# Performance work log

Measured on AMD Instinct MI355X. Metric: run time of the kernel, lower is better.

The kernel has to match this reference:

```python
import jax, jax.numpy as jnp
import numpy as np

SEQ, B, V, E, H, L = 64, 64, 32000, 512, 512, 2


def setup_inputs() -> dict:
    key = jax.random.key(0)
    ks = jax.random.split(key, 12)
    k = float(np.sqrt(1.0 / H))
    u = lambda kk, shape, a, b: jax.random.uniform(kk, shape, jnp.float32, a, b)
    return {
        "inputs": jax.random.randint(ks[0], (SEQ, B), 0, V),          # [T, B] token ids
        "hidden": jnp.zeros((L, B, H), jnp.float32),                   # initial hidden
        "emb": u(ks[1], (V, E), -0.1, 0.1),                            # embedding table
        "Wr_w": u(ks[2], (L, H, E + H), -k, k),                        # reset gate [L,H,2H]
        "Wr_b": u(ks[3], (L, H), -k, k),
        "Wz_w": u(ks[4], (L, H, E + H), -k, k),                        # update gate
        "Wz_b": u(ks[5], (L, H), -k, k),
        "Wh_w": u(ks[6], (L, H, E + H), -k, k),                        # candidate
        "Wh_b": u(ks[7], (L, H), -k, k),
        "out_w": u(ks[8], (V, H), -0.1, 0.1),                          # output projection
        "out_b": jnp.zeros((V,), jnp.float32),
    }


def reference(inputs, hidden, emb, Wr_w, Wr_b, Wz_w, Wz_b, Wh_w, Wh_b, out_w, out_b):
    # GRU recurrence over time via lax.scan (dropout disabled: dp_keep_prob=1.0)
    def step(h, tok):
        x = emb[tok]  # [B, E]
        new_h = []
        for i in range(L):  # fixed small layer loop
            hi = h[i]  # [B, H]
            cat = jnp.concatenate([x, hi], axis=1)  # [B, E+H]
            r = jax.nn.sigmoid(cat @ Wr_w[i].T + Wr_b[i])
            z = jax.nn.sigmoid(cat @ Wz_w[i].T + Wz_b[i])
            h_hat = jnp.tanh(jnp.concatenate([x, r * hi], axis=1) @ Wh_w[i].T + Wh_b[i])
            x = (1.0 - z) * hi + z * h_hat  # next layer input / new hidden
            new_h.append(x)
        logits_t = x @ out_w.T + out_b  # [B, V]
        return jnp.stack(new_h), logits_t

    hidden_final, logits = jax.lax.scan(step, hidden, inputs)
    return logits, hidden_final  # [T,B,V], [L,B,H]
```

## Files before the change

kernel.cpp:

```cpp
#include <hip/hip_runtime.h>

constexpr int NT = 64;
constexpr int NB = 64;
constexpr int NV = 32000;
constexpr int NE = 512;
constexpr int NH = 512;
constexpr int NPAIR = 16 * 250;

constexpr size_t SZ_OW  = (size_t)NV * NE;
constexpr size_t SZ_XE  = (size_t)NT * NB * NE;
constexpr size_t SZ_H   = (size_t)NB * NH;
constexpr size_t LOGITS = (size_t)NT * NB * NV;

typedef float f32x4 __attribute__((ext_vector_type(4)));
typedef int   i32x4 __attribute__((ext_vector_type(4)));
typedef short bf16x8 __attribute__((ext_vector_type(8)));
typedef short s16x4 __attribute__((ext_vector_type(4)));
typedef _Float16 f16x8 __attribute__((ext_vector_type(8)));

__device__ __forceinline__ unsigned short f2bf(float x) {
  unsigned u = __float_as_uint(x);
  u += 0x7FFFu + ((u >> 16) & 1u);
  return (unsigned short)(u >> 16);
}
__device__ __forceinline__ float bf2f(unsigned short s) {
  return __uint_as_float(((unsigned)s) << 16);
}
__device__ __forceinline__ void split2(float v, short* hi, short* lo) {
  unsigned short h = f2bf(v);
  *hi = (short)h;
  *lo = (short)f2bf(v - bf2f(h));
}
__device__ __forceinline__ f32x4 mma_bf16(bf16x8 a, bf16x8 b, f32x4 c) {
  return __builtin_amdgcn_mfma_f32_16x16x32_bf16(a, b, c, 0, 0, 0);
}
__device__ __forceinline__ f32x4 mma_f16(f16x8 a, f16x8 b, f32x4 c) {
  return __builtin_amdgcn_mfma_f32_16x16x32_f16(a, b, c, 0, 0, 0);
}
__device__ __forceinline__ float fast_sigmoid(float x) {
  return __builtin_amdgcn_rcpf(1.0f + __expf(-x));
}
__device__ __forceinline__ float fast_tanh(float x) {
  return 1.0f - 2.0f * __builtin_amdgcn_rcpf(1.0f + __expf(2.0f * x));
}

__device__ __forceinline__ void st_sc32u(unsigned* p, unsigned v) {
  asm volatile("global_store_dword %0, %1, off sc0 sc1" :: "v"(p), "v"(v) : "memory");
}
__device__ __forceinline__ void st_sc128(void* p, i32x4 v) {
  asm volatile("global_store_dwordx4 %0, %1, off sc0 sc1" :: "v"(p), "v"(v) : "memory");
}
__device__ __forceinline__ void st_nt(float* p, float v) {
  asm volatile("global_store_dword %0, %1, off nt" :: "v"(p), "v"(v) : "memory");
}
__device__ __forceinline__ unsigned ld_sc32u(const unsigned* p) {
  unsigned v;
  asm volatile("global_load_dword %0, %1, off sc0 sc1\n\ts_waitcnt vmcnt(0)"
               : "=v"(v) : "v"(p) : "memory");
  return v;
}

__device__ __forceinline__ void publish(unsigned* flags, int slot, unsigned val) {
  asm volatile("s_waitcnt vmcnt(0)" ::: "memory");
  __syncthreads();
  if (threadIdx.x == 0) st_sc32u(&flags[(size_t)slot * 32], val);
}

__global__ void k_prep(
    const float* __restrict__ outw, const int* __restrict__ toks,
    const float* __restrict__ emb, const float* __restrict__ hid,
    _Float16* OWf, short* XeHi, short* XeLo,
    short* X1Hi, short* X1Lo, short* h0Hi, short* h0Lo) {
  const size_t stride = (size_t)gridDim.x * blockDim.x;
  const size_t N1 = SZ_OW, N2 = N1 + SZ_XE, N3 = N2 + SZ_H, N4 = N3 + SZ_H;
  for (size_t x = (size_t)blockIdx.x * blockDim.x + threadIdx.x; x < N4; x += stride) {
    if (x < N1) {
      OWf[x] = (_Float16)outw[x];
    } else if (x < N2) {
      size_t p = x - N1;
      size_t r = p >> 9, c = p & 511u;
      int tok = toks[r];
      float v = emb[(size_t)tok * 512 + c];
      short hi, lo; split2(v, &hi, &lo);
      XeHi[p] = hi; XeLo[p] = lo;
    } else if (x < N3) {
      size_t p = x - N2;
      short hi, lo; split2(hid[p], &hi, &lo);
      h0Hi[p] = hi; h0Lo[p] = lo;
    } else {
      size_t p = x - N3;
      short hi, lo; split2(hid[SZ_H + p], &hi, &lo);
      X1Hi[p] = hi; X1Lo[p] = lo;
    }
  }
}

__device__ __forceinline__ void mmaP32(
    const short* __restrict__ aH, const short* __restrict__ aL, int base,
    const short* lsHi_, const short* lsLo_,
    f32x4 (&accH)[2], f32x4 (&accL)[2], int wave, int l15, int lq) {
  const int kq = wave >> 1, rhalf = wave & 1;
  const int r0 = rhalf * 16 + l15;
#pragma unroll
  for (int i = 0; i < 4; ++i) {
    const int ko = kq * 128 + i * 32 + lq * 8;
    const int kg = base + ko;
    const int e0 = (l15 * 1024 + kg) ^ ((l15 & 7) << 3);
    const int e1 = ((16 + l15) * 1024 + kg) ^ ((l15 & 7) << 3);
    bf16x8 bh0 = *(const bf16x8*)&lsHi_[e0];
    bf16x8 bl0 = *(const bf16x8*)&lsLo_[e0];
    bf16x8 bh1 = *(const bf16x8*)&lsHi_[e1];
    bf16x8 bl1 = *(const bf16x8*)&lsLo_[e1];
    bf16x8 ah = *(const bf16x8*)&aH[r0 * 512 + ko];
    bf16x8 al = *(const bf16x8*)&aL[r0 * 512 + ko];
    accH[0] = mma_bf16(ah, bh0, accH[0]);
    accH[1] = mma_bf16(ah, bh1, accH[1]);
    accL[0] = mma_bf16(al, bh0, accL[0]);
    accL[1] = mma_bf16(al, bh1, accL[1]);
    accL[0] = mma_bf16(ah, bl0, accL[0]);
    accL[1] = mma_bf16(ah, bl1, accL[1]);
  }
}
__device__ __forceinline__ void reduce4(float* lsRed_, f32x4 (&accH)[2], f32x4 (&accL)[2],
                                        f32x4 (&acc)[2], int wave, int l15, int lq) {
  const int kq = wave >> 1, rhalf = wave & 1;
  acc[0] = accH[0] + accL[0];
  acc[1] = accH[1] + accL[1];
  const int pos = l15 * 16 + lq * 4;
  if (kq) {
    *(f32x4*)&lsRed_[(((kq - 1) * 2 + rhalf) * 2 + 0) * 256 + pos] = acc[0];
    *(f32x4*)&lsRed_[(((kq - 1) * 2 + rhalf) * 2 + 1) * 256 + pos] = acc[1];
  }
  __syncthreads();
  if (!kq) {
#pragma unroll
    for (int s = 0; s < 3; ++s) {
      acc[0] += *(const f32x4*)&lsRed_[((s * 2 + rhalf) * 2 + 0) * 256 + pos];
      acc[1] += *(const f32x4*)&lsRed_[((s * 2 + rhalf) * 2 + 1) * 256 + pos];
    }
  }
  __syncthreads();
}

__device__ __forceinline__ void mmaD(
    const short* __restrict__ pAH, const short* __restrict__ pAL,
    int kloc0, int kkGlob0, const short* lsHi_, const short* lsLo_,
    f32x4 (&accH)[2], f32x4 (&accL)[2], int l15, int lq, int rhalf, int rowbase) {
  const int r0 = rowbase + rhalf * 16 + l15;
#pragma unroll 4
  for (int i = 0; i < 8; ++i) {
    const int kk = kkGlob0 + i * 32 + lq * 8;
    const int ka = kloc0 + i * 32 + lq * 8;
    const int e0 = (l15 * 1024 + kk) ^ ((l15 & 7) << 3);
    const int e1 = ((16 + l15) * 1024 + kk) ^ ((l15 & 7) << 3);
    bf16x8 bh0 = *(const bf16x8*)&lsHi_[e0];
    bf16x8 bl0 = *(const bf16x8*)&lsLo_[e0];
    bf16x8 bh1 = *(const bf16x8*)&lsHi_[e1];
    bf16x8 bl1 = *(const bf16x8*)&lsLo_[e1];
    bf16x8 ah = *(const bf16x8*)&pAH[r0 * 512 + ka];
    bf16x8 al = *(const bf16x8*)&pAL[r0 * 512 + ka];
    accH[0] = mma_bf16(ah, bh0, accH[0]);
    accH[1] = mma_bf16(ah, bh1, accH[1]);
    accL[0] = mma_bf16(al, bh0, accL[0]);
    accL[1] = mma_bf16(al, bh1, accL[1]);
    accL[0] = mma_bf16(ah, bl0, accL[0]);
    accL[1] = mma_bf16(ah, bl1, accL[1]);
  }
}
__device__ __forceinline__ void phaseD(
    const short* aLoH, const short* aLoL,
    const short* aHiH, const short* aHiL,
    const short* lsHi_, const short* lsLo_, float* lsRed_,
    f32x4 (&acc)[2], int wave, int l15, int lq, int rowbase) {
  const int khalf = wave >> 1, rhalf = wave & 1;
  f32x4 accH[2] = {}, accL[2] = {};
  const short* pAH = (khalf < 2) ? aLoH : aHiH;
  const short* pAL = (khalf < 2) ? aLoL : aHiL;
  mmaD(pAH, pAL, (khalf & 1) * 256, khalf * 256, lsHi_, lsLo_,
       accH, accL, l15, lq, rhalf, rowbase);
  acc[0] = accH[0] + accL[0];
  acc[1] = accH[1] + accL[1];
  const int pos = l15 * 16 + lq * 4;
  if (wave >= 2) {
    *(f32x4*)&lsRed_[((wave - 2) * 2 + 0) * 256 + pos] = acc[0];
    *(f32x4*)&lsRed_[((wave - 2) * 2 + 1) * 256 + pos] = acc[1];
  }
  __syncthreads();
  if (wave < 2) {
#pragma unroll
    for (int s = 0; s < 3; ++s) {
      const int slot = (wave & 1) + 2 * s;
      acc[0] += *(const f32x4*)&lsRed_[(slot * 2 + 0) * 256 + pos];
      acc[1] += *(const f32x4*)&lsRed_[(slot * 2 + 1) * 256 + pos];
    }
  }
  __syncthreads();
}

__device__ __forceinline__ void stage_weights(
    short* lsHi, short* lsLo, const float* srcBase0, const float* srcBase1,
    int jc, int tid) {
  for (int i = tid; i < 8192; i += 512) {
    const int j = i >> 8;
    const int k4 = (i & 255) << 2;
    const int g = jc + j;
    const float* src = (srcBase1 && g >= 512)
        ? (srcBase1 + (size_t)(g - 512) * 1024 + k4)
        : (srcBase0 + (size_t)g * 1024 + k4);
    f32x4 v = *(const f32x4*)src;
    s16x4 h4, l4;
#pragma unroll
    for (int q = 0; q < 4; ++q) { short hi, lo; split2(v[q], &hi, &lo); h4[q] = hi; l4[q] = lo; }
    const int els = (j * 1024 + k4) ^ ((j & 7) << 3);
    *(s16x4*)&lsHi[els] = h4;
    *(s16x4*)&lsLo[els] = l4;
  }
}

__device__ void gemm_loop(char* pool, int tid,
                          const _Float16* Af, const _Float16* Bw,
                          const float* bias, float* C,
                          unsigned* flags, unsigned* tcnt) {
  _Float16* lsA0 = (_Float16*)pool;
  _Float16* lsA1 = lsA0 + 128 * 64;
  _Float16* lsB  = lsA1 + 128 * 64;
  volatile int* bc = (volatile int*)(pool + 49152);
  const int wave = tid >> 6, lane = tid & 63, l15 = lane & 15, lq = lane >> 4;
  const int wr = (wave >> 2) * 64, wc = (wave & 3) * 32;
  unsigned lastR = 0;
  __syncthreads();
  for (;;) {
    if (tid == 0)
      *bc = (int)__hip_atomic_fetch_add(tcnt, 1u, __ATOMIC_RELAXED,
                                        __HIP_MEMORY_SCOPE_AGENT);
    __syncthreads();
    const int pr = *bc;
    __syncthreads();
    if (pr >= NPAIR) break;
    const int p = pr / 250, bn = pr - p * 250;
    const unsigned Rneed = 4u * (unsigned)p + 4u;
    if (lastR < Rneed) {
      if (tid < 32) {
        const unsigned* fp = &flags[(size_t)(160 + tid) * 32];
        while (ld_sc32u(fp) < Rneed) __builtin_amdgcn_s_sleep(8);
      }
      lastR = Rneed;
    }
    __syncthreads();
    f32x4 acc0[4][2] = {}, acc1[4][2] = {};
    const size_t arow0 = (size_t)p * 256;
    const size_t brow0 = (size_t)bn * 128;
    for (int kb = 0; kb < 512; kb += 64) {
#pragma unroll
      for (int i = 0; i < 2; ++i) {
        int c = tid + i * 512;
        int row = c >> 3, kc = (c & 7) * 8;
        int el = (row * 64 + kc) ^ ((row & 7) << 3);
        *(f16x8*)&lsA0[el] = *(const f16x8*)(Af + (arow0 + row) * 512 + kb + kc);
        *(f16x8*)&lsA1[el] = *(const f16x8*)(Af + (arow0 + 128 + row) * 512 + kb + kc);
        *(f16x8*)&lsB[el]  = *(const f16x8*)(Bw + (brow0 + row) * 512 + kb + kc);
      }
      __syncthreads();
#pragma unroll
      for (int k0 = 0; k0 < 64; k0 += 32) {
        const int kk = k0 + lq * 8;
        f16x8 af0[4], af1[4], bfr[2];
#pragma unroll
        for (int i = 0; i < 4; ++i) {
          int ra = wr + i * 16 + l15;
          int el = (ra * 64 + kk) ^ ((ra & 7) << 3);
          af0[i] = *(const f16x8*)&lsA0[el];
          af1[i] = *(const f16x8*)&lsA1[el];
        }
#pragma unroll
        for (int jt = 0; jt < 2; ++jt) {
          int rb = wc + jt * 16 + l15;
          bfr[jt] = *(const f16x8*)&lsB[(rb * 64 + kk) ^ ((rb & 7) << 3)];
        }
#pragma unroll
        for (int i = 0; i < 4; ++i)
#pragma unroll
          for (int jt = 0; jt < 2; ++jt) {
            acc0[i][jt] = mma_f16(af0[i], bfr[jt], acc0[i][jt]);
            acc1[i][jt] = mma_f16(af1[i], bfr[jt], acc1[i][jt]);
          }
      }
      __syncthreads();
    }
#pragma unroll
    for (int i = 0; i < 4; ++i) {
#pragma unroll
      for (int jt = 0; jt < 2; ++jt) {
        const size_t col = brow0 + wc + jt * 16 + l15;
        const float bval = bias[col];
#pragma unroll
        for (int r = 0; r < 4; ++r) {
          const size_t row = arow0 + wr + i * 16 + lq * 4 + r;
          st_nt(&C[row * (size_t)NV + col], acc0[i][jt][r] + bval);
          st_nt(&C[(row + 128) * (size_t)NV + col], acc1[i][jt][r] + bval);
        }
      }
    }
  }
}

__launch_bounds__(512, 1)
__global__ void k_main(
    const float* __restrict__ Wr, const float* __restrict__ Wz, const float* __restrict__ Wh,
    const float* __restrict__ Wrb, const float* __restrict__ Wzb, const float* __restrict__ Whb,
    const short* __restrict__ XeHi, const short* __restrict__ XeLo,
    short* X1Hi, short* X1Lo, _Float16* X1f16,
    short* h0Hi, short* h0Lo,
    short* rh0Hi, short* rh0Lo, short* rh1Hi, short* rh1Lo,
    float* z0, float* z1, float* hidOut,
    const _Float16* OWf, const float* outb, float* out,
    unsigned* flags, unsigned* tcnt) {
  __shared__ __align__(16) char pool[153600];
  short* lsHi = (short*)pool;
  short* lsLo = lsHi + 32 * 1024;
  float* lsRed = (float*)(pool + 131072);
  short* sH    = (short*)(pool + 131072);
  short* sL    = sH + 1024;
  float* sZA   = (float*)(pool + 131072);
  short* stH   = (short*)(pool + 143360);
  short* stL   = stH + 1024;
  float* sZ    = (float*)(pool + 147456);
  _Float16* sX = (_Float16*)(pool + 151552);

  const int wg = blockIdx.x;
  const int tid = threadIdx.x;
  const int wave = tid >> 6, lane = tid & 63, l15 = lane & 15, lq = lane >> 4;

  if (wg < 64) {
    const int cg = wg >> 1, rh = wg & 1, jc = cg * 32, rowbase = rh * 32;
    const bool isR = (jc < 512);
    stage_weights(lsHi, lsLo, Wr, Wz, jc, tid);
    float biasL0, biasL1;
    {
      const int j0 = jc + l15, j1 = j0 + 16;
      biasL0 = (j0 < 512) ? Wrb[j0] : Wzb[j0 - 512];
      biasL1 = (j1 < 512) ? Wrb[j1] : Wzb[j1 - 512];
    }
    __syncthreads();
    for (int t = 0; t < NT; ++t) {
      f32x4 accH[2] = {}, accL[2] = {};
      mmaP32(XeHi + (size_t)t * SZ_H + rowbase * 512,
             XeLo + (size_t)t * SZ_H + rowbase * 512, 0,
             lsHi, lsLo, accH, accL, wave, l15, lq);
      if (tid < 16) {
        const unsigned* fp = &flags[(size_t)(128 + tid * 2 + rh) * 32];
        while (ld_sc32u(fp) < (unsigned)t) {}
      }
      __syncthreads();
      const short* hH = h0Hi + (size_t)t * SZ_H + rowbase * 512;
      const short* hL = h0Lo + (size_t)t * SZ_H + rowbase * 512;
      i32x4 pre;
      const int pbuf = tid >> 7, pq = tid & 127, prow = pq >> 2, pc = pq & 3;
      if (isR && tid < 256)
        pre = *(const i32x4*)((pbuf ? hL : hH) + prow * 512 + jc + pc * 8);
      mmaP32(hH, hL, 512, lsHi, lsLo, accH, accL, wave, l15, lq);
      if (isR && tid < 256)
        *(i32x4*)&(pbuf ? stL : stH)[prow * 32 + pc * 8] = pre;
      f32x4 acc[2];
      reduce4(lsRed, accH, accL, acc, wave, l15, lq);
      if (wave < 2) {
#pragma unroll
        for (int ct = 0; ct < 2; ++ct) {
          const int jj = ct * 16 + l15;
          const float bv = ct ? biasL1 : biasL0;
#pragma unroll
          for (int r = 0; r < 4; ++r) {
            const int lb = wave * 16 + lq * 4 + r;
            const float s = fast_sigmoid(acc[ct][r] + bv);
            if (isR) {
              const float hv = bf2f((unsigned short)stH[lb * 32 + jj]) +
                               bf2f((unsigned short)stL[lb * 32 + jj]);
              short hi, lo; split2(s * hv, &hi, &lo);
              sH[lb * 32 + jj] = hi; sL[lb * 32 + jj] = lo;
            } else {
              sZA[lb * 32 + jj] = s;
            }
          }
        }
      }
      __syncthreads();
      if (isR) {
        if (tid < 256) {
          i32x4 v = *(const i32x4*)&(pbuf ? sL : sH)[prow * 32 + pc * 8];
          st_sc128((pbuf ? rh0Lo : rh0Hi) + (size_t)t * SZ_H +
                   (size_t)(rowbase + prow) * 512 + jc + pc * 8, v);
        }
      } else {
        if (tid < 256) {
          const int row = tid >> 3, c = tid & 7;
          i32x4 v = *(const i32x4*)&sZA[row * 32 + c * 4];
          st_sc128(z0 + (size_t)t * SZ_H + (size_t)(rowbase + row) * 512 +
                   (jc - 512) + c * 4, v);
        }
      }
      publish(flags, wg, (unsigned)(t + 1));
    }
  } else if (wg < 128) {
    const int idx = wg - 64, cg = idx >> 1, rh = idx & 1, jc = cg * 32, rowbase = rh * 32;
    const bool isR = (jc < 512);
    stage_weights(lsHi, lsLo, Wr + (size_t)512 * 1024, Wz + (size_t)512 * 1024, jc, tid);
    float biasL0, biasL1;
    {
      const int j0 = jc + l15, j1 = j0 + 16;
      biasL0 = (j0 < 512) ? Wrb[512 + j0] : Wzb[512 + j0 - 512];
      biasL1 = (j1 < 512) ? Wrb[512 + j1] : Wzb[512 + j1 - 512];
    }
    __syncthreads();
    for (int t = 0; t < NT; ++t) {
      if (tid < 16) {
        const unsigned* fp = &flags[(size_t)(128 + tid * 2 + rh) * 32];
        while (ld_sc32u(fp) < (unsigned)(t + 1)) {}
      } else if (tid >= 64 && tid < 80) {
        const unsigned* fp = &flags[(size_t)(160 + (tid - 64) * 2 + rh) * 32];
        while (ld_sc32u(fp) < (unsigned)t) {}
      }
      __syncthreads();
      const short* xH = h0Hi + (size_t)(t + 1) * SZ_H;
      const short* xL = h0Lo + (size_t)(t + 1) * SZ_H;
      const short* hH = X1Hi + (size_t)t * SZ_H;
      const short* hL = X1Lo + (size_t)t * SZ_H;
      i32x4 pre;
      const int pbuf = tid >> 7, pq = tid & 127, prow = pq >> 2, pc = pq & 3;
      if (isR && tid < 256)
        pre = *(const i32x4*)((pbuf ? hL : hH) +
                              (size_t)(rowbase + prow) * 512 + jc + pc * 8);
      f32x4 acc[2];
      phaseD(xH, xL, hH, hL, lsHi, lsLo, lsRed, acc, wave, l15, lq, rowbase);
      if (isR && tid < 256)
        *(i32x4*)&(pbuf ? stL : stH)[prow * 32 + pc * 8] = pre;
      __syncthreads();
      if (wave < 2) {
#pragma unroll
        for (int ct = 0; ct < 2; ++ct) {
          const int jj = ct * 16 + l15;
          const float bv = ct ? biasL1 : biasL0;
#pragma unroll
          for (int r = 0; r < 4; ++r) {
            const int lb = wave * 16 + lq * 4 + r;
            const float s = fast_sigmoid(acc[ct][r] + bv);
            if (isR) {
              const float hv = bf2f((unsigned short)stH[lb * 32 + jj]) +
                               bf2f((unsigned short)stL[lb * 32 + jj]);
              short hi, lo; split2(s * hv, &hi, &lo);
              sH[lb * 32 + jj] = hi; sL[lb * 32 + jj] = lo;
            } else {
              sZA[lb * 32 + jj] = s;
            }
          }
        }
      }
      __syncthreads();
      if (isR) {
        if (tid < 256) {
          i32x4 v = *(const i32x4*)&(pbuf ? sL : sH)[prow * 32 + pc * 8];
          st_sc128((pbuf ? rh1Lo : rh1Hi) + (size_t)t * SZ_H +
                   (size_t)(rowbase + prow) * 512 + jc + pc * 8, v);
        }
      } else {
        if (tid < 256) {
          const int row = tid >> 3, c = tid & 7;
          i32x4 v = *(const i32x4*)&sZA[row * 32 + c * 4];
          st_sc128(z1 + (size_t)t * SZ_H + (size_t)(rowbase + row) * 512 +
                   (jc - 512) + c * 4, v);
        }
      }
      publish(flags, wg, (unsigned)(t + 1));
    }
  } else if (wg < 192) {
    const bool isL1 = (wg >= 160);
    const int idx = isL1 ? (wg - 160) : (wg - 128);
    const int cg = idx >> 1, rh = idx & 1, jc = cg * 32, rowbase = rh * 32;
    const int layer = isL1 ? 1 : 0;
    stage_weights(lsHi, lsLo, Wh + (size_t)layer * 512 * 1024, nullptr, jc, tid);
    const float biasL0 = Whb[layer * 512 + jc + l15];
    const float biasL1 = Whb[layer * 512 + jc + 16 + l15];
    __syncthreads();
    short* myHi = isL1 ? X1Hi : h0Hi;
    short* myLo = isL1 ? X1Lo : h0Lo;
    const short* rhHi_ = isL1 ? rh1Hi : rh0Hi;
    const short* rhLo_ = isL1 ? rh1Lo : rh0Lo;
    const float* zArr = isL1 ? z1 : z0;
    const int fbase = isL1 ? 64 : 0;
    for (int t = 0; t < NT; ++t) {
      const int pbuf = tid >> 7, pq = tid & 127, prow = pq >> 2, pc = pq & 3;
      if (tid < 256) {
        const short* src = (pbuf ? myLo : myHi) + (size_t)t * SZ_H +
                           (size_t)(rowbase + prow) * 512 + jc + pc * 8;
        *(i32x4*)&(pbuf ? stL : stH)[prow * 32 + pc * 8] = *(const i32x4*)src;
      }
      f32x4 accH[2] = {}, accL[2] = {};
      if (isL1) {
        if (tid < 16) {
          const unsigned* fp = &flags[(size_t)(128 + tid * 2 + rh) * 32];
          while (ld_sc32u(fp) < (unsigned)(t + 1)) {}
        }
        __syncthreads();
        mmaP32(h0Hi + (size_t)(t + 1) * SZ_H + rowbase * 512,
               h0Lo + (size_t)(t + 1) * SZ_H + rowbase * 512, 0,
               lsHi, lsLo, accH, accL, wave, l15, lq);
      } else {
        mmaP32(XeHi + (size_t)t * SZ_H + rowbase * 512,
               XeLo + (size_t)t * SZ_H + rowbase * 512, 0,
               lsHi, lsLo, accH, accL, wave, l15, lq);
      }
      if (tid < 32) {
        const unsigned* fp = &flags[(size_t)(fbase + tid * 2 + rh) * 32];
        while (ld_sc32u(fp) < (unsigned)(t + 1)) {}
      }
      __syncthreads();
      f32x4 zv;
      const int zrow = tid >> 3, zc = tid & 7;
      if (tid < 256)
        zv = *(const f32x4*)(zArr + (size_t)t * SZ_H +
                             (size_t)(rowbase + zrow) * 512 + jc + zc * 4);
      mmaP32(rhHi_ + (size_t)t * SZ_H + rowbase * 512,
             rhLo_ + (size_t)t * SZ_H + rowbase * 512, 512,
             lsHi, lsLo, accH, accL, wave, l15, lq);
      if (tid < 256)
        *(f32x4*)&sZ[zrow * 32 + zc * 4] = zv;
      f32x4 acc[2];
      reduce4(lsRed, accH, accL, acc, wave, l15, lq);
      if (wave < 2) {
#pragma unroll
        for (int ct = 0; ct < 2; ++ct) {
          const int jj = ct * 16 + l15, j = jc + jj;
          const float bv = ct ? biasL1 : biasL0;
#pragma unroll
          for (int r = 0; r < 4; ++r) {
            const int lb = wave * 16 + lq * 4 + r;
            const float hh = fast_tanh(acc[ct][r] + bv);
            const float z = sZ[lb * 32 + jj];
            const float ho = bf2f((unsigned short)stH[lb * 32 + jj]) +
                             bf2f((unsigned short)stL[lb * 32 + jj]);
            const float hn = (1.0f - z) * ho + z * hh;
            short hi, lo; split2(hn, &hi, &lo);
            sH[lb * 32 + jj] = hi; sL[lb * 32 + jj] = lo;
            if (isL1) sX[lb * 32 + jj] = (_Float16)hn;
            if (t == NT - 1)
              hidOut[(size_t)layer * SZ_H + (size_t)(rowbase + lb) * 512 + j] = hn;
          }
        }
      }
      __syncthreads();
      if (tid < 256) {
        i32x4 v = *(const i32x4*)&(pbuf ? sL : sH)[prow * 32 + pc * 8];
        st_sc128((pbuf ? myLo : myHi) + (size_t)(t + 1) * SZ_H +
                 (size_t)(rowbase + prow) * 512 + jc + pc * 8, v);
      } else if (isL1 && tid < 384) {
        const int q = tid - 256, row = q >> 2, c = q & 3;
        i32x4 v = *(const i32x4*)&sX[row * 32 + c * 8];
        st_sc128(X1f16 + (size_t)t * SZ_H + (size_t)(rowbase + row) * 512 + jc + c * 8, v);
      }
      publish(flags, wg, (unsigned)(t + 1));
    }
  }
  gemm_loop(pool, tid, X1f16, OWf, outb, out, flags, tcnt);
}

extern "C" void kernel_launch(void* const* d_in, const int* in_sizes, int n_in,
                              void* d_out, int out_size, void* d_ws, size_t ws_size,
                              hipStream_t stream) {
  (void)in_sizes; (void)n_in; (void)out_size; (void)ws_size;
  const int*   toks = (const int*)d_in[0];
  const float* hid  = (const float*)d_in[1];
  const float* emb  = (const float*)d_in[2];
  const float* Wr   = (const float*)d_in[3];
  const float* Wrb  = (const float*)d_in[4];
  const float* Wz   = (const float*)d_in[5];
  const float* Wzb  = (const float*)d_in[6];
  const float* Wh   = (const float*)d_in[7];
  const float* Whb  = (const float*)d_in[8];
  const float* outw = (const float*)d_in[9];
  const float* outb = (const float*)d_in[10];
  float* out = (float*)d_out;

  char* base = (char*)d_ws;
  size_t off = 0;
  auto carve = [&](size_t bytes) -> char* {
    char* r = base + off;
    off = (off + bytes + 255) & ~(size_t)255;
    return r;
  };
  _Float16* OWf   = (_Float16*)carve(SZ_OW * 2);
  short*    XeHi  = (short*)carve(SZ_XE * 2);
  short*    XeLo  = (short*)carve(SZ_XE * 2);
  short*    X1Hi  = (short*)carve((size_t)(NT + 1) * SZ_H * 2);
  short*    X1Lo  = (short*)carve((size_t)(NT + 1) * SZ_H * 2);
  _Float16* X1f16 = (_Float16*)carve((size_t)NT * SZ_H * 2);
  short*    h0Hi  = (short*)carve((size_t)(NT + 1) * SZ_H * 2);
  short*    h0Lo  = (short*)carve((size_t)(NT + 1) * SZ_H * 2);
  short*    rh0Hi = (short*)carve((size_t)NT * SZ_H * 2);
  short*    rh0Lo = (short*)carve((size_t)NT * SZ_H * 2);
  short*    rh1Hi = (short*)carve((size_t)NT * SZ_H * 2);
  short*    rh1Lo = (short*)carve((size_t)NT * SZ_H * 2);
  float*    z0    = (float*)carve((size_t)NT * SZ_H * 4);
  float*    z1    = (float*)carve((size_t)NT * SZ_H * 4);
  unsigned* flags = (unsigned*)carve(32768);
  unsigned* tcnt  = (unsigned*)carve(256);

  hipMemsetAsync(flags, 0, 32768, stream);
  hipMemsetAsync(tcnt, 0, 256, stream);

  k_prep<<<2048, 256, 0, stream>>>(outw, toks, emb, hid,
                                   OWf, XeHi, XeLo, X1Hi, X1Lo, h0Hi, h0Lo);

  k_main<<<256, 512, 0, stream>>>(
      Wr, Wz, Wh, Wrb, Wzb, Whb, XeHi, XeLo,
      X1Hi, X1Lo, X1f16, h0Hi, h0Lo,
      rh0Hi, rh0Lo, rh1Hi, rh1Lo, z0, z1,
      out + LOGITS, OWf, outb, out, flags, tcnt);
}
```

Baseline: 724.8 us.

## Replace block-wide flag waits with per-wave polling of only needed producer flags

In the persistent GRU kernel, the cross-workgroup dependency waits previously had a few threads spin on all producer flags and then hit a __syncthreads barrier. Now each wave polls only the subset of flags for the K-slice it consumes, using a wave-wide __all vote. Each prefetch thread waits on the single flag for its own column chunk. This removes block barriers and lets waves start their MMA slices as soon as their own inputs are ready. The logits epilogue also hoists the bias loads out of the loop. The cost is more polling traffic on the flags and subtler memory-ordering assumptions between waves.

```diff
diff --git a/kernel.cpp b/kernel.cpp
--- a/kernel.cpp
+++ b/kernel.cpp
@@ -58,6 +58,20 @@
   asm volatile("global_load_dword %0, %1, off sc0 sc1\n\ts_waitcnt vmcnt(0)"
                : "=v"(v) : "v"(p) : "memory");
   return v;
+}
+
+__device__ __forceinline__ void wait1(const unsigned* flags, int slot, unsigned thr) {
+  while (ld_sc32u(&flags[(size_t)slot * 32]) < thr) {}
+}
+__device__ __forceinline__ void wave_poll4(const unsigned* flags, int slotBase, int cgBase,
+                                           int rh, unsigned thr, int lane) {
+  const unsigned* fp = &flags[(size_t)(slotBase + (cgBase + (lane & 3)) * 2 + rh) * 32];
+  while (!__all((int)(ld_sc32u(fp) >= thr))) {}
+}
+__device__ __forceinline__ void wave_poll8(const unsigned* flags, int slotBase, int cgBase,
+                                           int rh, unsigned thr, int lane) {
+  const unsigned* fp = &flags[(size_t)(slotBase + (cgBase + (lane & 7)) * 2 + rh) * 32];
+  while (!__all((int)(ld_sc32u(fp) >= thr))) {}
 }
 
 __device__ __forceinline__ void publish(unsigned* flags, int slot, unsigned val) {
@@ -167,17 +181,8 @@
     accL[1] = mma_bf16(ah, bl1, accL[1]);
   }
 }
-__device__ __forceinline__ void phaseD(
-    const short* aLoH, const short* aLoL,
-    const short* aHiH, const short* aHiL,
-    const short* lsHi_, const short* lsLo_, float* lsRed_,
-    f32x4 (&acc)[2], int wave, int l15, int lq, int rowbase) {
-  const int khalf = wave >> 1, rhalf = wave & 1;
-  f32x4 accH[2] = {}, accL[2] = {};
-  const short* pAH = (khalf < 2) ? aLoH : aHiH;
-  const short* pAL = (khalf < 2) ? aLoL : aHiL;
-  mmaD(pAH, pAL, (khalf & 1) * 256, khalf * 256, lsHi_, lsLo_,
-       accH, accL, l15, lq, rhalf, rowbase);
+__device__ __forceinline__ void reduceD(float* lsRed_, f32x4 (&accH)[2], f32x4 (&accL)[2],
+                                        f32x4 (&acc)[2], int wave, int l15, int lq) {
   acc[0] = accH[0] + accL[0];
   acc[1] = accH[1] + accL[1];
   const int pos = l15 * 16 + lq * 4;
@@ -287,18 +292,19 @@
       }
       __syncthreads();
     }
+    const float b0v = bias[brow0 + wc + l15];
+    const float b1v = bias[brow0 + wc + 16 + l15];
 #pragma unroll
     for (int i = 0; i < 4; ++i) {
 #pragma unroll
-      for (int jt = 0; jt < 2; ++jt) {
-        const size_t col = brow0 + wc + jt * 16 + l15;
-        const float bval = bias[col];
-#pragma unroll
-        for (int r = 0; r < 4; ++r) {
-          const size_t row = arow0 + wr + i * 16 + lq * 4 + r;
-          st_nt(&C[row * (size_t)NV + col], acc0[i][jt][r] + bval);
-          st_nt(&C[(row + 128) * (size_t)NV + col], acc1[i][jt][r] + bval);
-        }
+      for (int r = 0; r < 4; ++r) {
+        const size_t row = arow0 + wr + i * 16 + lq * 4 + r;
+        float* pa = C + row * (size_t)NV + brow0 + wc + l15;
+        st_nt(pa, acc0[i][0][r] + b0v);
+        st_nt(pa + 16, acc0[i][1][r] + b1v);
+        float* pb = pa + (size_t)128 * NV;
+        st_nt(pb, acc1[i][0][r] + b0v);
+        st_nt(pb + 16, acc1[i][1][r] + b1v);
       }
     }
   }
@@ -347,17 +353,15 @@
       mmaP32(XeHi + (size_t)t * SZ_H + rowbase * 512,
              XeLo + (size_t)t * SZ_H + rowbase * 512, 0,
              lsHi, lsLo, accH, accL, wave, l15, lq);
-      if (tid < 16) {
-        const unsigned* fp = &flags[(size_t)(128 + tid * 2 + rh) * 32];
-        while (ld_sc32u(fp) < (unsigned)t) {}
-      }
-      __syncthreads();
       const short* hH = h0Hi + (size_t)t * SZ_H + rowbase * 512;
       const short* hL = h0Lo + (size_t)t * SZ_H + rowbase * 512;
       i32x4 pre;
       const int pbuf = tid >> 7, pq = tid & 127, prow = pq >> 2, pc = pq & 3;
-      if (isR && tid < 256)
+      if (isR && tid < 256) {
+        wait1(flags, 128 + ((jc >> 5) * 2 + rh), (unsigned)t);
         pre = *(const i32x4*)((pbuf ? hL : hH) + prow * 512 + jc + pc * 8);
+      }
+      wave_poll4(flags, 128, 4 * (wave >> 1), rh, (unsigned)t, lane);
       mmaP32(hH, hL, 512, lsHi, lsLo, accH, accL, wave, l15, lq);
       if (isR && tid < 256)
         *(i32x4*)&(pbuf ? stL : stH)[prow * 32 + pc * 8] = pre;
@@ -412,28 +416,31 @@
     }
     __syncthreads();
     for (int t = 0; t < NT; ++t) {
-      if (tid < 16) {
-        const unsigned* fp = &flags[(size_t)(128 + tid * 2 + rh) * 32];
-        while (ld_sc32u(fp) < (unsigned)(t + 1)) {}
-      } else if (tid >= 64 && tid < 80) {
-        const unsigned* fp = &flags[(size_t)(160 + (tid - 64) * 2 + rh) * 32];
-        while (ld_sc32u(fp) < (unsigned)t) {}
-      }
-      __syncthreads();
       const short* xH = h0Hi + (size_t)(t + 1) * SZ_H;
       const short* xL = h0Lo + (size_t)(t + 1) * SZ_H;
       const short* hH = X1Hi + (size_t)t * SZ_H;
       const short* hL = X1Lo + (size_t)t * SZ_H;
       i32x4 pre;
       const int pbuf = tid >> 7, pq = tid & 127, prow = pq >> 2, pc = pq & 3;
-      if (isR && tid < 256)
+      if (isR && tid < 256) {
+        wait1(flags, 160 + ((jc >> 5) * 2 + rh), (unsigned)t);
         pre = *(const i32x4*)((pbuf ? hL : hH) +
                               (size_t)(rowbase + prow) * 512 + jc + pc * 8);
-      f32x4 acc[2];
-      phaseD(xH, xL, hH, hL, lsHi, lsLo, lsRed, acc, wave, l15, lq, rowbase);
+      }
+      f32x4 accH[2] = {}, accL[2] = {};
+      {
+        const int khalf = wave >> 1, rhalf = wave & 1;
+        if (khalf < 2) wave_poll8(flags, 128, (khalf & 1) * 8, rh, (unsigned)(t + 1), lane);
+        else           wave_poll8(flags, 160, (khalf & 1) * 8, rh, (unsigned)t, lane);
+        const short* pAH = (khalf < 2) ? xH : hH;
+        const short* pAL = (khalf < 2) ? xL : hL;
+        mmaD(pAH, pAL, (khalf & 1) * 256, khalf * 256, lsHi, lsLo,
+             accH, accL, l15, lq, rhalf, rowbase);
+      }
       if (isR && tid < 256)
         *(i32x4*)&(pbuf ? stL : stH)[prow * 32 + pc * 8] = pre;
-      __syncthreads();
+      f32x4 acc[2];
+      reduceD(lsRed, accH, accL, acc, wave, l15, lq);
       if (wave < 2) {
 #pragma unroll
         for (int ct = 0; ct < 2; ++ct) {
@@ -495,11 +502,7 @@
       }
       f32x4 accH[2] = {}, accL[2] = {};
       if (isL1) {
-        if (tid < 16) {
-          const unsigned* fp = &flags[(size_t)(128 + tid * 2 + rh) * 32];
-          while (ld_sc32u(fp) < (unsigned)(t + 1)) {}
-        }
-        __syncthreads();
+        wave_poll4(flags, 128, 4 * (wave >> 1), rh, (unsigned)(t + 1), lane);
         mmaP32(h0Hi + (size_t)(t + 1) * SZ_H + rowbase * 512,
                h0Lo + (size_t)(t + 1) * SZ_H + rowbase * 512, 0,
                lsHi, lsLo, accH, accL, wave, l15, lq);
@@ -508,16 +511,14 @@
                XeLo + (size_t)t * SZ_H + rowbase * 512, 0,
                lsHi, lsLo, accH, accL, wave, l15, lq);
       }
-      if (tid < 32) {
-        const unsigned* fp = &flags[(size_t)(fbase + tid * 2 + rh) * 32];
-        while (ld_sc32u(fp) < (unsigned)(t + 1)) {}
-      }
-      __syncthreads();
       f32x4 zv;
       const int zrow = tid >> 3, zc = tid & 7;
-      if (tid < 256)
+      if (tid < 256) {
+        wait1(flags, fbase + ((16 + (jc >> 5)) * 2 + rh), (unsigned)(t + 1));
         zv = *(const f32x4*)(zArr + (size_t)t * SZ_H +
                              (size_t)(rowbase + zrow) * 512 + jc + zc * 4);
+      }
+      wave_poll4(flags, fbase, 4 * (wave >> 1), rh, (unsigned)(t + 1), lane);
       mmaP32(rhHi_ + (size_t)t * SZ_H + rowbase * 512,
              rhLo_ + (size_t)t * SZ_H + rowbase * 512, 512,
              lsHi, lsLo, accH, accL, wave, l15, lq);
```

Result: faster. 698.4 us (-3.6%).
